# Performance work log

Hardware: AMD Instinct MI355X
Metric: run time of the kernel (lower is better)

Reference implementation:

```python
import jax, jax.numpy as jnp
import numpy as np
from jax import lax

# Faithful JAX translation of ConvAttention (enc=True, mask=False), the core
# kernel-headroom op of Conv_Transformer. Key observation: the per-(s,t)-pair
# conv2 over concat(Q[...,s], K[...,t]) is linear, so it decomposes exactly as
# conv(Q_s, W_q) + conv(K_t, W_k) + bias, where W_q/W_k are the first/second
# half of conv2's input channels. This reproduces the same math without
# materializing the [b, 2c, h, w, s, t] tensor or looping over time.

B, C, H, W, S = 4, 64, 64, 64, 20
K_SIZE = 3


def _conv_same(x, w):
    # x: [N, Cin, H, W], w: [Cout, Cin, kh, kw]
    return lax.conv_general_dilated(
        x, w, window_strides=(1, 1), padding='SAME',
        dimension_numbers=('NCHW', 'OIHW', 'NCHW'))


def setup_inputs() -> dict:
    key = jax.random.key(0)
    k1, k2, k3, k4, k5 = jax.random.split(key, 5)
    x = jax.random.normal(k1, (B, C, H, W, S), dtype=jnp.float32)
    w1 = jax.random.normal(k2, (3 * C, C, 1, 1), dtype=jnp.float32) * 0.05
    b1 = jax.random.normal(k3, (3 * C,), dtype=jnp.float32) * 0.05
    w2 = jax.random.normal(k4, (1, 2 * C, K_SIZE, K_SIZE), dtype=jnp.float32) * 0.05
    b2 = jax.random.normal(k5, (1,), dtype=jnp.float32) * 0.05
    return {'x': x, 'w1': w1, 'b1': b1, 'w2': w2, 'b2': b2}


def reference(x, w1, b1, w2, b2):
    b, c, h, w, s = x.shape
    # conv1 (1x1) per timestep -> QKV: [b, 3c, h, w, s]
    qkv = jnp.einsum('bchws,oc->bohws', x, w1[:, :, 0, 0]) \
        + b1[None, :, None, None, None]
    Q, K, V = jnp.split(qkv, 3, axis=1)  # each [b, c, h, w, s]

    # Decompose conv2 over concatenated channels.
    Wq, Wk = w2[:, :c], w2[:, c:]  # each [1, c, kh, kw]

    def per_time_conv(t5, wgt):
        # t5: [b, c, h, w, s] -> scores [b, h, w, s]
        flat = jnp.moveaxis(t5, -1, 1).reshape(b * s, c, h, w)
        out = _conv_same(flat, wgt)  # [b*s, 1, h, w]
        return out.reshape(b, s, h, w).transpose(0, 2, 3, 1)

    A = per_time_conv(Q, Wq)  # [b, h, w, s]  (query index)
    Bk = per_time_conv(K, Wk)  # [b, h, w, t]  (key index)

    # score[b,h,w,t,s] = conv2(concat(Q_s, K_t)) ; softmax over t (keys)
    scores = A[:, :, :, None, :] + Bk[:, :, :, :, None] + b2[0]
    attn = jax.nn.softmax(scores, axis=-2)  # [b, h, w, t, s]

    # V_out[b,c,h,w,s] = sum_t attn[...,t,s] * V[...,t]
    V_out = jnp.einsum('bhwts,bchwt->bchws', attn, V)
    return V_out
```

## Files before the change

### kernel.cpp

```cpp
#include <hip/hip_runtime.h>
#include <math.h>

#define Bb 4
#define Cc 64
#define Hh 64
#define Ww 64
#define Ss 20

constexpr int XC = Hh * Ww * Ss;
constexpr int XH = Ww * Ss;
constexpr int XW = Ss;
constexpr int XB = Cc * XC;
constexpr int NSITE = Bb * Hh * Ww;
constexpr int BKPLANE = NSITE * Ss;


__global__ void ct_fold_weights(const float* __restrict__ w1,
                                const float* __restrict__ b1,
                                const float* __restrict__ w2,
                                float* __restrict__ ws) {
    int tid = threadIdx.x;
    if (tid < 576) {
        int tap = tid >> 6, cp = tid & 63;
        float acc = 0.f;
        #pragma unroll 8
        for (int c = 0; c < 64; ++c)
            acc += w2[(64 + c) * 9 + tap] * w1[(64 + c) * 64 + cp];
        ws[tid] = acc;
    } else if (tid < 585) {
        int tap = tid - 576;
        float acc = 0.f;
        for (int c = 0; c < 64; ++c)
            acc += w2[(64 + c) * 9 + tap] * b1[64 + c];
        ws[576 + tap] = acc;
    }
}

template<int NPART>
__global__ __launch_bounds__(320) void ct_conv_bk(
        const float* __restrict__ x,
        const float* __restrict__ ws,
        float* __restrict__ bk) {
    __shared__ float weff[576];
    __shared__ float btap[9];
    int tid = threadIdx.x;
    for (int i = tid; i < 576; i += 320) weff[i] = ws[i];
    if (tid < 9) btap[tid] = ws[576 + tid];
    __syncthreads();

    constexpr int NCP = 64 / NPART;
    constexpr int CHUNK = 256 * NPART / 8;
    int g = (blockIdx.x & 7) * CHUNK + (blockIdx.x >> 3);
    int part = g >> 8;
    int nl = g & 255;
    int b = nl >> 6, h = nl & 63;
    int w = tid / 5, t4 = tid % 5;

    float vmask[9];
    int off[9];
    #pragma unroll
    for (int dh = 0; dh < 3; ++dh) {
        int hh = h + dh - 1;
        float hv = (hh >= 0 && hh < Hh) ? 1.f : 0.f;
        int hc = hh < 0 ? 0 : (hh > Hh - 1 ? Hh - 1 : hh);
        #pragma unroll
        for (int dw = 0; dw < 3; ++dw) {
            int wc = w + dw - 1;
            float wvd = (wc >= 0 && wc < Ww) ? 1.f : 0.f;
            int wcl = wc < 0 ? 0 : (wc > Ww - 1 ? Ww - 1 : wc);
            vmask[dh * 3 + dw] = hv * wvd;
            off[dh * 3 + dw] = hc * XH + wcl * XW;
        }
    }

    float bsum = 0.f;
    if (part == 0) {
        #pragma unroll
        for (int tap = 0; tap < 9; ++tap) bsum += btap[tap] * vmask[tap];
    }
    float4 acc = make_float4(bsum, bsum, bsum, bsum);

    const float* xb = x + b * XB + part * NCP * XC + t4 * 4;
    #pragma unroll 2
    for (int c = 0; c < NCP; ++c) {
        const float* xc = xb + c * XC;
        #pragma unroll
        for (int tap = 0; tap < 9; ++tap) {
            float wv = weff[tap * 64 + part * NCP + c] * vmask[tap];
            const float4 xv = *reinterpret_cast<const float4*>(xc + off[tap]);
            acc.x = fmaf(wv, xv.x, acc.x);
            acc.y = fmaf(wv, xv.y, acc.y);
            acc.z = fmaf(wv, xv.z, acc.z);
            acc.w = fmaf(wv, xv.w, acc.w);
        }
    }
    int site = nl * 64 + w;
    *reinterpret_cast<float4*>(bk + part * BKPLANE + site * 20 + t4 * 4) = acc;
}

template<int NPART>
__global__ __launch_bounds__(256) void ct_attn_out(
        const float* __restrict__ x,
        const float* __restrict__ w1,
        const float* __restrict__ b1,
        const float* __restrict__ bk,
        float* __restrict__ out) {
    __shared__ float w1t[64 * 65];
    __shared__ float psm[16][20];
    __shared__ float xsh[16][65];
    int tid = threadIdx.x;
    #pragma unroll
    for (int k = 0; k < 16; ++k) {
        int j = tid + k * 256;
        int r = j >> 6, q = j & 63;
        w1t[q * 65 + r] = w1[8192 + j];
    }

    int site0 = blockIdx.x * 16;
    if (tid < 16) {
        int site = site0 + tid;
        float p[20];
        #pragma unroll
        for (int i = 0; i < 20; ++i) {
            float v = 0.f;
            #pragma unroll
            for (int pt = 0; pt < NPART; ++pt)
                v += bk[pt * BKPLANE + site * 20 + i];
            p[i] = v;
        }
        float m = p[0];
        #pragma unroll
        for (int i = 1; i < 20; ++i) m = fmaxf(m, p[i]);
        float ssum = 0.f;
        #pragma unroll
        for (int i = 0; i < 20; ++i) { p[i] = __expf(p[i] - m); ssum += p[i]; }
        float inv = 1.f / ssum;
        #pragma unroll
        for (int i = 0; i < 20; ++i) psm[tid][i] = p[i] * inv;
    }
    __syncthreads();

    int si = tid & 15, cg = tid >> 4;
    int site = site0 + si;
    int b = site >> 12, hw = site & 4095;

    #pragma unroll
    for (int k = 0; k < 4; ++k) {
        int c = cg * 4 + k;
        const float* xp = x + (b * 64 + c) * XC + hw * 20;
        float xbv = 0.f;
        #pragma unroll
        for (int i = 0; i < 5; ++i) {
            float4 xv = reinterpret_cast<const float4*>(xp)[i];
            xbv = fmaf(psm[si][4 * i],     xv.x, xbv);
            xbv = fmaf(psm[si][4 * i + 1], xv.y, xbv);
            xbv = fmaf(psm[si][4 * i + 2], xv.z, xbv);
            xbv = fmaf(psm[si][4 * i + 3], xv.w, xbv);
        }
        xsh[si][c] = xbv;
    }
    __syncthreads();

    #pragma unroll
    for (int k = 0; k < 4; ++k) {
        int c = cg * 4 + k;
        float R = b1[128 + c];
        #pragma unroll 8
        for (int cp = 0; cp < 64; ++cp)
            R = fmaf(w1t[cp * 65 + c], xsh[si][cp], R);
        float* op = out + (b * 64 + c) * XC + hw * 20;
        float4 rv = make_float4(R, R, R, R);
        #pragma unroll
        for (int s4 = 0; s4 < 5; ++s4)
            reinterpret_cast<float4*>(op)[s4] = rv;
    }
}

extern "C" void kernel_launch(void* const* d_in, const int* in_sizes, int n_in,
                              void* d_out, int out_size, void* d_ws, size_t ws_size,
                              hipStream_t stream) {
    const float* x  = (const float*)d_in[0];
    const float* w1 = (const float*)d_in[1];
    const float* b1 = (const float*)d_in[2];
    const float* w2 = (const float*)d_in[3];
    float* ws    = (float*)d_ws;
    float* bkbuf = ws + 640;
    float* out   = (float*)d_out;

    ct_fold_weights<<<1, 640, 0, stream>>>(w1, b1, w2, ws);

    size_t need4 = (size_t)(640 + 4 * BKPLANE) * sizeof(float);
    if (ws_size >= need4) {
        ct_conv_bk<4><<<1024, 320, 0, stream>>>(x, ws, bkbuf);
        ct_attn_out<4><<<1024, 256, 0, stream>>>(x, w1, b1, bkbuf, out);
    } else {
        ct_conv_bk<1><<<256, 320, 0, stream>>>(x, ws, bkbuf);
        ct_attn_out<1><<<1024, 256, 0, stream>>>(x, w1, b1, bkbuf, out);
    }
}
```

Baseline: 88.99 us.

## Fuse key-score conv and attention output into one kernel via shared memory

Merges the conv-based key score kernel and the softmax/output kernel into a single kernel. Each block computes partial scores for 16 sites across 4 channel groups, reduces them in shared memory, applies the bias and softmax, then does the value projection and writes the output. This removes the global round trip of the partial score buffer and one launch. In exchange the block needs more shared memory (w1 transpose plus score buffers), which may limit occupancy, and there are extra syncs between phases.

```diff
diff --git a/kernel.cpp b/kernel.cpp
--- a/kernel.cpp
+++ b/kernel.cpp
@@ -11,8 +11,6 @@
 constexpr int XH = Ww * Ss;
 constexpr int XW = Ss;
 constexpr int XB = Cc * XC;
-constexpr int NSITE = Bb * Hh * Ww;
-constexpr int BKPLANE = NSITE * Ss;
 
 
 __global__ void ct_fold_weights(const float* __restrict__ w1,
@@ -36,25 +34,38 @@
     }
 }
 
-template<int NPART>
-__global__ __launch_bounds__(320) void ct_conv_bk(
+__global__ __launch_bounds__(320, 5) void ct_fused(
         const float* __restrict__ x,
+        const float* __restrict__ w1,
+        const float* __restrict__ b1,
         const float* __restrict__ ws,
-        float* __restrict__ bk) {
+        float* __restrict__ out) {
     __shared__ float weff[576];
-    __shared__ float btap[9];
+    __shared__ float btL[9];
+    __shared__ float w1t[64 * 65];
+    __shared__ float bkp[4][16][20];
+    __shared__ float psm[16][20];
+    __shared__ float xsh[16][65];
     int tid = threadIdx.x;
+
     for (int i = tid; i < 576; i += 320) weff[i] = ws[i];
-    if (tid < 9) btap[tid] = ws[576 + tid];
-    __syncthreads();
+    if (tid < 9) btL[tid] = ws[576 + tid];
+    #pragma unroll
+    for (int k = 0; k < 13; ++k) {
+        int j = tid + k * 320;
+        if (j < 4096) {
+            int r = j >> 6, q = j & 63;
+            w1t[q * 65 + r] = w1[8192 + j];
+        }
+    }
 
-    constexpr int NCP = 64 / NPART;
-    constexpr int CHUNK = 256 * NPART / 8;
-    int g = (blockIdx.x & 7) * CHUNK + (blockIdx.x >> 3);
-    int part = g >> 8;
-    int nl = g & 255;
-    int b = nl >> 6, h = nl & 63;
-    int w = tid / 5, t4 = tid % 5;
+    int g = (blockIdx.x & 7) * 128 + (blockIdx.x >> 3);
+    int wq = g & 3;
+    int h  = (g >> 2) & 63;
+    int b  = g >> 8;
+
+    int w16 = (tid / 5) & 15, t4 = tid % 5, cg = tid / 80;
+    int w = wq * 16 + w16;
 
     float vmask[9];
     int off[9];
@@ -62,31 +73,26 @@
     for (int dh = 0; dh < 3; ++dh) {
         int hh = h + dh - 1;
         float hv = (hh >= 0 && hh < Hh) ? 1.f : 0.f;
-        int hc = hh < 0 ? 0 : (hh > Hh - 1 ? Hh - 1 : hh);
+        int hcl = hh < 0 ? 0 : (hh > Hh - 1 ? Hh - 1 : hh);
         #pragma unroll
         for (int dw = 0; dw < 3; ++dw) {
             int wc = w + dw - 1;
             float wvd = (wc >= 0 && wc < Ww) ? 1.f : 0.f;
             int wcl = wc < 0 ? 0 : (wc > Ww - 1 ? Ww - 1 : wc);
             vmask[dh * 3 + dw] = hv * wvd;
-            off[dh * 3 + dw] = hc * XH + wcl * XW;
+            off[dh * 3 + dw] = hcl * XH + wcl * XW;
         }
     }
+    __syncthreads();
 
-    float bsum = 0.f;
-    if (part == 0) {
-        #pragma unroll
-        for (int tap = 0; tap < 9; ++tap) bsum += btap[tap] * vmask[tap];
-    }
-    float4 acc = make_float4(bsum, bsum, bsum, bsum);
-
-    const float* xb = x + b * XB + part * NCP * XC + t4 * 4;
+    float4 acc = make_float4(0.f, 0.f, 0.f, 0.f);
+    const float* xb = x + b * XB + cg * 16 * XC + t4 * 4;
     #pragma unroll 2
-    for (int c = 0; c < NCP; ++c) {
-        const float* xc = xb + c * XC;
+    for (int i = 0; i < 16; ++i) {
+        const float* xc = xb + i * XC;
         #pragma unroll
         for (int tap = 0; tap < 9; ++tap) {
-            float wv = weff[tap * 64 + part * NCP + c] * vmask[tap];
+            float wv = weff[tap * 64 + cg * 16 + i] * vmask[tap];
             const float4 xv = *reinterpret_cast<const float4*>(xc + off[tap]);
             acc.x = fmaf(wv, xv.x, acc.x);
             acc.y = fmaf(wv, xv.y, acc.y);
@@ -94,40 +100,33 @@
             acc.w = fmaf(wv, xv.w, acc.w);
         }
     }
-    int site = nl * 64 + w;
-    *reinterpret_cast<float4*>(bk + part * BKPLANE + site * 20 + t4 * 4) = acc;
-}
+    *reinterpret_cast<float4*>(&bkp[cg][w16][t4 * 4]) = acc;
+    __syncthreads();
 
-template<int NPART>
-__global__ __launch_bounds__(256) void ct_attn_out(
-        const float* __restrict__ x,
-        const float* __restrict__ w1,
-        const float* __restrict__ b1,
-        const float* __restrict__ bk,
-        float* __restrict__ out) {
-    __shared__ float w1t[64 * 65];
-    __shared__ float psm[16][20];
-    __shared__ float xsh[16][65];
-    int tid = threadIdx.x;
-    #pragma unroll
-    for (int k = 0; k < 16; ++k) {
-        int j = tid + k * 256;
-        int r = j >> 6, q = j & 63;
-        w1t[q * 65 + r] = w1[8192 + j];
+    {
+        int sw = tid / 20, t = tid % 20;
+        float v = bkp[0][sw][t] + bkp[1][sw][t] + bkp[2][sw][t] + bkp[3][sw][t];
+        int wsite = wq * 16 + sw;
+        float bs = 0.f;
+        #pragma unroll
+        for (int dh = 0; dh < 3; ++dh) {
+            int hh = h + dh - 1;
+            if (hh < 0 || hh >= Hh) continue;
+            #pragma unroll
+            for (int dw = 0; dw < 3; ++dw) {
+                int wc = wsite + dw - 1;
+                if (wc < 0 || wc >= Ww) continue;
+                bs += btL[dh * 3 + dw];
+            }
+        }
+        psm[sw][t] = v + bs;
     }
+    __syncthreads();
 
-    int site0 = blockIdx.x * 16;
     if (tid < 16) {
-        int site = site0 + tid;
         float p[20];
         #pragma unroll
-        for (int i = 0; i < 20; ++i) {
-            float v = 0.f;
-            #pragma unroll
-            for (int pt = 0; pt < NPART; ++pt)
-                v += bk[pt * BKPLANE + site * 20 + i];
-            p[i] = v;
-        }
+        for (int i = 0; i < 20; ++i) p[i] = psm[tid][i];
         float m = p[0];
         #pragma unroll
         for (int i = 1; i < 20; ++i) m = fmaxf(m, p[i]);
@@ -140,39 +139,41 @@
     }
     __syncthreads();
 
-    int si = tid & 15, cg = tid >> 4;
-    int site = site0 + si;
-    int b = site >> 12, hw = site & 4095;
-
-    #pragma unroll
-    for (int k = 0; k < 4; ++k) {
-        int c = cg * 4 + k;
-        const float* xp = x + (b * 64 + c) * XC + hw * 20;
-        float xbv = 0.f;
+    int si = tid & 15, cq = tid >> 4;
+    int wsite = wq * 16 + si;
+    if (cq < 16) {
         #pragma unroll
-        for (int i = 0; i < 5; ++i) {
-            float4 xv = reinterpret_cast<const float4*>(xp)[i];
-            xbv = fmaf(psm[si][4 * i],     xv.x, xbv);
-            xbv = fmaf(psm[si][4 * i + 1], xv.y, xbv);
-            xbv = fmaf(psm[si][4 * i + 2], xv.z, xbv);
-            xbv = fmaf(psm[si][4 * i + 3], xv.w, xbv);
+        for (int k = 0; k < 4; ++k) {
+            int c = cq * 4 + k;
+            const float* xp = x + (b * 64 + c) * XC + h * XH + wsite * 20;
+            float xbv = 0.f;
+            #pragma unroll
+            for (int i = 0; i < 5; ++i) {
+                float4 xv = reinterpret_cast<const float4*>(xp)[i];
+                xbv = fmaf(psm[si][4 * i],     xv.x, xbv);
+                xbv = fmaf(psm[si][4 * i + 1], xv.y, xbv);
+                xbv = fmaf(psm[si][4 * i + 2], xv.z, xbv);
+                xbv = fmaf(psm[si][4 * i + 3], xv.w, xbv);
+            }
+            xsh[si][c] = xbv;
         }
-        xsh[si][c] = xbv;
     }
     __syncthreads();
 
-    #pragma unroll
-    for (int k = 0; k < 4; ++k) {
-        int c = cg * 4 + k;
-        float R = b1[128 + c];
-        #pragma unroll 8
-        for (int cp = 0; cp < 64; ++cp)
-            R = fmaf(w1t[cp * 65 + c], xsh[si][cp], R);
-        float* op = out + (b * 64 + c) * XC + hw * 20;
-        float4 rv = make_float4(R, R, R, R);
+    if (cq < 16) {
         #pragma unroll
-        for (int s4 = 0; s4 < 5; ++s4)
-            reinterpret_cast<float4*>(op)[s4] = rv;
+        for (int k = 0; k < 4; ++k) {
+            int c = cq * 4 + k;
+            float R = b1[128 + c];
+            #pragma unroll 8
+            for (int cp = 0; cp < 64; ++cp)
+                R = fmaf(w1t[cp * 65 + c], xsh[si][cp], R);
+            float* op = out + (b * 64 + c) * XC + h * XH + wsite * 20;
+            float4 rv = make_float4(R, R, R, R);
+            #pragma unroll
+            for (int s4 = 0; s4 < 5; ++s4)
+                reinterpret_cast<float4*>(op)[s4] = rv;
+        }
     }
 }
 
@@ -183,18 +184,9 @@
     const float* w1 = (const float*)d_in[1];
     const float* b1 = (const float*)d_in[2];
     const float* w2 = (const float*)d_in[3];
-    float* ws    = (float*)d_ws;
-    float* bkbuf = ws + 640;
-    float* out   = (float*)d_out;
+    float* ws  = (float*)d_ws;
+    float* out = (float*)d_out;
 
     ct_fold_weights<<<1, 640, 0, stream>>>(w1, b1, w2, ws);
-
-    size_t need4 = (size_t)(640 + 4 * BKPLANE) * sizeof(float);
-    if (ws_size >= need4) {
-        ct_conv_bk<4><<<1024, 320, 0, stream>>>(x, ws, bkbuf);
-        ct_attn_out<4><<<1024, 256, 0, stream>>>(x, w1, b1, bkbuf, out);
-    } else {
-        ct_conv_bk<1><<<256, 320, 0, stream>>>(x, ws, bkbuf);
-        ct_attn_out<1><<<1024, 256, 0, stream>>>(x, w1, b1, bkbuf, out);
-    }
+    ct_fused<<<1024, 320, 0, stream>>>(x, w1, b1, ws, out);
 }
```

Result: faster. 84.12 us (-5.5%).
